# Kernel tuning notes

Hardware: AMD Instinct MI355X
Metric: run time of the kernel (lower is better)

## Reference

```python
import jax, jax.numpy as jnp
import numpy as np

DIM = 512
NUM_HEADS = 8
HEAD_DIM = DIM // NUM_HEADS
SCALE = HEAD_DIM ** -0.5
B, T = 8, 1024


def setup_inputs() -> dict:
    key = jax.random.key(0)
    ks = jax.random.split(key, 6)
    x = jax.random.normal(ks[0], (B, T, DIM), dtype=jnp.float32)
    attn_mask = jax.random.randint(ks[1], (B, T, T), 0, 2) == 1  # bool [B,T,T]
    s = 1.0 / np.sqrt(DIM)
    qkv_w = jax.random.uniform(ks[2], (3 * DIM, DIM), jnp.float32, -s, s)
    qkv_b = jax.random.uniform(ks[3], (3 * DIM,), jnp.float32, -s, s)
    proj_w = jax.random.uniform(ks[4], (DIM, DIM), jnp.float32, -s, s)
    proj_b = jax.random.uniform(ks[5], (DIM,), jnp.float32, -s, s)
    return {"x": x, "attn_mask": attn_mask, "qkv_w": qkv_w, "qkv_b": qkv_b,
            "proj_w": proj_w, "proj_b": proj_b}


def reference(x, attn_mask, qkv_w, qkv_b, proj_w, proj_b):
    b, t, c = x.shape
    # QKV projection (torch Linear: x @ W.T + b), split into q,k,v heads
    qkv = x @ qkv_w.T + qkv_b                      # [b,t,3*c]
    qkv = qkv.reshape(b, t, 3, NUM_HEADS, HEAD_DIM)
    qkv = jnp.transpose(qkv, (2, 0, 3, 1, 4))      # [3,b,h,t,d]
    q, k, v = qkv[0], qkv[1], qkv[2]
    scores = jnp.einsum('bhqd,bhkd->bhqk', q, k) * SCALE  # [b,h,t,t]
    min_val = jnp.finfo(scores.dtype).min
    scores = jnp.where(attn_mask[:, None, :, :], min_val, scores)
    attn = jax.nn.softmax(scores, axis=-1)
    out = jnp.einsum('bhqk,bhkd->bhqd', attn, v)   # [b,h,t,d]
    out = jnp.transpose(out, (0, 2, 1, 3)).reshape(b, t, c)
    return out @ proj_w.T + proj_b
```

## Files before the change

kernel.cpp:

```cpp
#include <hip/hip_runtime.h>
#include <math.h>

#define DIM   512
#define NH    8
#define HD    64
#define BATCH 8
#define SEQ   1024
#define QSCALE 0.18033688011112042f

typedef unsigned short u16;
typedef unsigned int   u32;
typedef unsigned long long u64;
typedef __bf16 bf16x8 __attribute__((ext_vector_type(8)));
typedef float  f32x4  __attribute__((ext_vector_type(4)));

__device__ inline u16 f2bf(float f) {
  u32 u = __builtin_bit_cast(u32, f);
  return (u16)((u + 0x7fffu + ((u >> 16) & 1u)) >> 16);
}
__device__ inline float bf2f(u16 h) {
  return __builtin_bit_cast(float, (u32)h << 16);
}
__device__ inline u32 pk2(float a, float b) {
  return (u32)f2bf(a) | ((u32)f2bf(b) << 16);
}

__device__ inline void a16(const u16* g, u16* l) {
  __builtin_amdgcn_global_load_lds(
      (const __attribute__((address_space(1))) u32*)g,
      (__attribute__((address_space(3))) u32*)l, 16, 0, 0);
}


__device__ inline void decomp_body(const float* __restrict__ src, u16* ph,
                                   u16* pl, int t) {
  #pragma unroll
  for (int c = 0; c < 4; ++c) {
    const int cid = c * 256 + t;
    const int row = cid & 15, kc = cid >> 4;
    float f[8];
    *(float4*)&f[0] = *(const float4*)&src[row * DIM + kc * 8];
    *(float4*)&f[4] = *(const float4*)&src[row * DIM + kc * 8 + 4];
    u16 hv[8], lv[8];
    #pragma unroll
    for (int j = 0; j < 8; ++j) {
      hv[j] = f2bf(f[j]);
      lv[j] = f2bf(f[j] - bf2f(hv[j]));
    }
    *(uint4*)&ph[(size_t)cid * 8] = *(const uint4*)hv;
    *(uint4*)&pl[(size_t)cid * 8] = *(const uint4*)lv;
  }
}

__global__ __launch_bounds__(256) void prep(
    const int* __restrict__ mask, u64* __restrict__ bits,
    const float* __restrict__ x, u16* __restrict__ xhi, u16* __restrict__ xlo,
    const float* __restrict__ qkvw, u16* __restrict__ wqh, u16* __restrict__ wql,
    const float* __restrict__ projw, u16* __restrict__ wph, u16* __restrict__ wpl) {
  const int blk = blockIdx.x;
  const int t = threadIdx.x;
  if (blk < 32768) {
    const size_t gid = (size_t)blk * 256 + t;
    const int lane = t & 63;
    const size_t w = gid >> 6;
    const int v = mask[w * 64 + lane];
    const u64 b = __ballot(v != 0);
    if (lane == 0) {
      const int bb = (int)(w >> 14), q = (int)((w >> 4) & 1023),
                kt = (int)(w & 15);
      bits[(((size_t)(bb << 4 | kt)) << 10) | q] = b;
    }
  } else if (blk < 33280) {
    const int rg = blk - 32768;
    decomp_body(x + (size_t)rg * 16 * DIM, xhi + (size_t)rg * 8192,
                xlo + (size_t)rg * 8192, t);
  } else if (blk < 33376) {
    const int rg = blk - 33280;
    decomp_body(qkvw + (size_t)rg * 16 * DIM, wqh + (size_t)rg * 8192,
                wql + (size_t)rg * 8192, t);
  } else {
    const int rg = blk - 33376;
    decomp_body(projw + (size_t)rg * 16 * DIM, wph + (size_t)rg * 8192,
                wpl + (size_t)rg * 8192, t);
  }
}

template <bool QKV>
__global__ __launch_bounds__(256) void mfma_gemm(
    const u16* __restrict__ Agh, const u16* __restrict__ Agl,
    const u16* __restrict__ Bgh, const u16* __restrict__ Bgl,
    const float* __restrict__ bias, void* __restrict__ out0,
    u16* __restrict__ kfr, u16* __restrict__ vfr) {
  __shared__ u16 sAh[4096];
  __shared__ u16 sAl[4096];
  __shared__ u16 sBh[4096];
  __shared__ u16 sBl[4096];

  const int tid = threadIdx.x;
  const int lane = tid & 63;
  const int wv = tid >> 6;
  const int lk = lane & 15, lq = lane >> 4;
  const int m0 = blockIdx.x * 128, n0 = blockIdx.y * 128;
  const int wm = (wv & 1) * 4;
  const int wn = (wv >> 1) * 4;

  const u16* gAh = Agh + (size_t)(m0 >> 4) * 8192 + lane * 8;
  const u16* gAl = Agl + (size_t)(m0 >> 4) * 8192 + lane * 8;
  const u16* gBh = Bgh + (size_t)(n0 >> 4) * 8192 + lane * 8;
  const u16* gBl = Bgl + (size_t)(n0 >> 4) * 8192 + lane * 8;

  f32x4 acc[4][4];
  #pragma unroll
  for (int i = 0; i < 4; ++i)
    #pragma unroll
    for (int j = 0; j < 4; ++j) acc[i][j] = (f32x4){0.f, 0.f, 0.f, 0.f};

  #pragma unroll 1
  for (int ki = 0; ki < 16; ++ki) {
    __syncthreads();
    #pragma unroll
    for (int it = 0; it < 2; ++it) {
      const int t = it * 4 + wv;
      const size_t go = (size_t)t * 8192 + ki * 512;
      const int lo_ = t * 512 + lane * 8;
      a16(gAh + go, &sAh[lo_]);
      a16(gAl + go, &sAl[lo_]);
      a16(gBh + go, &sBh[lo_]);
      a16(gBl + go, &sBl[lo_]);
    }
    __syncthreads();

    bf16x8 ah[4], al[4], bh[4], bl[4];
    #pragma unroll
    for (int i = 0; i < 4; ++i) {
      ah[i] = *(const bf16x8*)&sAh[(wm + i) * 512 + lane * 8];
      al[i] = *(const bf16x8*)&sAl[(wm + i) * 512 + lane * 8];
      bh[i] = *(const bf16x8*)&sBh[(wn + i) * 512 + lane * 8];
      bl[i] = *(const bf16x8*)&sBl[(wn + i) * 512 + lane * 8];
    }
    #pragma unroll
    for (int i = 0; i < 4; ++i)
      #pragma unroll
      for (int j = 0; j < 4; ++j) {
        acc[i][j] = __builtin_amdgcn_mfma_f32_16x16x32_bf16(ah[i], bh[j], acc[i][j], 0, 0, 0);
        acc[i][j] = __builtin_amdgcn_mfma_f32_16x16x32_bf16(ah[i], bl[j], acc[i][j], 0, 0, 0);
        acc[i][j] = __builtin_amdgcn_mfma_f32_16x16x32_bf16(al[i], bh[j], acc[i][j], 0, 0, 0);
      }
  }

  #pragma unroll
  for (int j = 0; j < 4; ++j) {
    const int n = n0 + (wn + j) * 16 + lk;
    const float bv_ = bias[n];
    #pragma unroll
    for (int i = 0; i < 4; ++i) {
      const int mb = m0 + (wm + i) * 16 + lq * 4;
      if (QKV) {
        const int which = n >> 9, h = (n >> 6) & 7, d = n & 63;
        const int b = mb >> 10, tok0 = mb & 1023;
        const size_t hb = (size_t)((b << 3) + h) << 16;
        if (which == 2) {
          const size_t base = hb + ((size_t)(tok0 >> 6) << 12) +
                              ((size_t)((d >> 4) & 3) << 10) +
                              ((size_t)((tok0 >> 5) & 1) << 9) +
                              ((size_t)((d & 15) + (((tok0 >> 3) & 3) << 4)) << 3) +
                              (size_t)(tok0 & 7);
          uint2 o2;
          o2.x = pk2(acc[i][j][0] + bv_, acc[i][j][1] + bv_);
          o2.y = pk2(acc[i][j][2] + bv_, acc[i][j][3] + bv_);
          *(uint2*)&vfr[base] = o2;
        } else if (which == 1) {
          const size_t base = hb + ((size_t)(tok0 >> 4) << 10) +
                              ((size_t)(d >> 5) << 9) + (size_t)(d & 7) +
                              ((size_t)(((d >> 3) & 3) << 4) << 3);
          #pragma unroll
          for (int r = 0; r < 4; ++r)
            kfr[base + (((tok0 & 15) + r) << 3)] = f2bf(acc[i][j][r] + bv_);
        } else {
          u16* dst = (u16*)out0;
          #pragma unroll
          for (int r = 0; r < 4; ++r)
            dst[(((size_t)((b << 3) + h) << 10 | (tok0 + r)) << 6) + d] =
                f2bf((acc[i][j][r] + bv_) * QSCALE);
        }
      } else {
        #pragma unroll
        for (int r = 0; r < 4; ++r)
          ((float*)out0)[(size_t)(mb + r) * DIM + n] = acc[i][j][r] + bv_;
      }
    }
  }
}

__global__ __launch_bounds__(256) void attn_mfma(
    const u16* __restrict__ qg, const u16* __restrict__ kfr,
    const u16* __restrict__ vfr, const u64* __restrict__ bitsT,
    u16* __restrict__ ohi, u16* __restrict__ olo) {
  __shared__ u16 Kls[4096];
  __shared__ u16 Vls[4096];
  __shared__ u16 Ps[64 * 72];

  const int tid = threadIdx.x;
  const int lane = tid & 63;
  const int wv = tid >> 6;
  const int lk = lane & 15, lq = lane >> 4;
  const int bh = blockIdx.x;
  const int q0 = blockIdx.y * 64;
  const int bb = bh >> 3;
  const int q = q0 + wv * 16 + lk;

  const u16* qrow = qg + ((size_t)(bh << 10 | q) << 6);
  const bf16x8 bq0 = *(const bf16x8*)(qrow + lq * 8);
  const bf16x8 bq1 = *(const bf16x8*)(qrow + 32 + lq * 8);

  const u16* kh = kfr + ((size_t)bh << 16);
  const u16* vh = vfr + ((size_t)bh << 16);
  const u64* bitp = bitsT + ((size_t)bb << 14) + q;
  u16* pw = &Ps[(wv * 16 + lk) * 72];

  f32x4 o_[4];
  float l = 0.f;
  #pragma unroll
  for (int t = 0; t < 4; ++t) o_[t] = (f32x4){0.f, 0.f, 0.f, 0.f};

  #pragma unroll 1
  for (int kt = 0; kt < 16; ++kt) {
    __syncthreads();
    #pragma unroll
    for (int it = 0; it < 2; ++it) {
      const int c = it * 4 + wv;
      const int off = c * 512 + lane * 8;
      a16(kh + (size_t)(kt << 12) + off, &Kls[off]);
      a16(vh + (size_t)(kt << 12) + off, &Vls[off]);
    }
    const u64 wd = bitp[kt << 10];
    __syncthreads();

    f32x4 st[4];
    const f32x4 z4 = (f32x4){0.f, 0.f, 0.f, 0.f};
    #pragma unroll
    for (int t = 0; t < 4; ++t) {
      const bf16x8 ak0 = *(const bf16x8*)&Kls[t * 1024 + lane * 8];
      const bf16x8 ak1 = *(const bf16x8*)&Kls[t * 1024 + 512 + lane * 8];
      f32x4 a = __builtin_amdgcn_mfma_f32_16x16x32_bf16(ak0, bq0, z4, 0, 0, 0);
      st[t] = __builtin_amdgcn_mfma_f32_16x16x32_bf16(ak1, bq1, a, 0, 0, 0);
    }

    const u32 w0 = (u32)wd, w1 = (u32)(wd >> 32);
    #pragma unroll
    for (int t = 0; t < 4; ++t) {
      const u32 w = (t < 2) ? w0 : w1;
      const int base = (t & 1) * 16 + lq * 4;
      float p[4];
      #pragma unroll
      for (int r = 0; r < 4; ++r) {
        const float sv = ((w >> (base + r)) & 1u) ? -INFINITY : st[t][r];
        p[r] = __builtin_amdgcn_exp2f(sv);
        l += p[r];
      }
      *(uint2*)(pw + t * 16 + lq * 4) = uint2{pk2(p[0], p[1]), pk2(p[2], p[3])};
    }

    const bf16x8 pa0 = *(const bf16x8*)(pw + lq * 8);
    const bf16x8 pa1 = *(const bf16x8*)(pw + 32 + lq * 8);
    #pragma unroll
    for (int t = 0; t < 4; ++t) {
      const bf16x8 vb0 = *(const bf16x8*)&Vls[t * 1024 + lane * 8];
      const bf16x8 vb1 = *(const bf16x8*)&Vls[t * 1024 + 512 + lane * 8];
      o_[t] = __builtin_amdgcn_mfma_f32_16x16x32_bf16(pa0, vb0, o_[t], 0, 0, 0);
      o_[t] = __builtin_amdgcn_mfma_f32_16x16x32_bf16(pa1, vb1, o_[t], 0, 0, 0);
    }
  }

  l += __shfl_xor(l, 16);
  l += __shfl_xor(l, 32);

  const int h = bh & 7;
  #pragma unroll
  for (int r = 0; r < 4; ++r) {
    const float inv = 1.0f / __shfl(l, lq * 4 + r);
    const int tok = q0 + wv * 16 + lq * 4 + r;
    const int m = (bb << 10) | tok;
    const size_t rgo = (size_t)(m >> 4) * 8192 + (size_t)(m & 15) * 8;
    #pragma unroll
    for (int t = 0; t < 4; ++t) {
      const int d = t * 16 + lk;
      const int k = (h << 6) | d;
      const float v = o_[t][r] * inv;
      const u16 hv = f2bf(v);
      const size_t off = rgo + (size_t)(k >> 3) * 128 + (k & 7);
      ohi[off] = hv;
      olo[off] = f2bf(v - bf2f(hv));
    }
  }
}

extern "C" void kernel_launch(void* const* d_in, const int* in_sizes, int n_in,
                              void* d_out, int out_size, void* d_ws,
                              size_t ws_size, hipStream_t stream) {
  const float* x      = (const float*)d_in[0];
  const int*   mask   = (const int*)d_in[1];
  const float* qkv_w  = (const float*)d_in[2];
  const float* qkv_b  = (const float*)d_in[3];
  const float* proj_w = (const float*)d_in[4];
  const float* proj_b = (const float*)d_in[5];
  float* out = (float*)d_out;

  const size_t SZ = (size_t)BATCH * NH * SEQ * HD;
  u64* bits = (u64*)d_ws;
  u16* qb  = (u16*)(bits + 131072);
  u16* kfr = qb + SZ;
  u16* vfr = kfr + SZ;
  u16* xhi = vfr + SZ;
  u16* xlo = xhi + SZ;
  u16* ohi = xlo + SZ;
  u16* olo = ohi + SZ;
  u16* wqh = olo + SZ;
  u16* wql = wqh + 1536 * 512;
  u16* wph = wql + 1536 * 512;
  u16* wpl = wph + 512 * 512;

  prep<<<33408, 256, 0, stream>>>(mask, bits, x, xhi, xlo,
                                  qkv_w, wqh, wql, proj_w, wph, wpl);
  mfma_gemm<true><<<dim3(64, 12), 256, 0, stream>>>(
      xhi, xlo, wqh, wql, qkv_b, qb, kfr, vfr);
  attn_mfma<<<dim3(64, SEQ / 64), 256, 0, stream>>>(
      qb, kfr, vfr, bits, ohi, olo);
  mfma_gemm<false><<<dim3(64, 4), 256, 0, stream>>>(
      ohi, olo, wph, wpl, proj_b, out, nullptr, nullptr);
}
```

Baseline: 214.6 us.

## Double-buffer LDS tiles in GEMM and attention kernels to overlap loads

Both the split-bf16 GEMM and the attention kernel now use two LDS buffers and prefetch the next K-tile while computing on the current one. This removes one barrier per iteration and hides global-to-LDS latency behind the MFMA work. MFMA sections are also wrapped in s_setprio so matrix work is favoured across waves. LDS use doubles (64KB in the GEMM), which may cut the number of resident blocks per CU, and the attention kernel now holds more fragments in registers.

```diff
diff --git a/kernel.cpp b/kernel.cpp
--- a/kernel.cpp
+++ b/kernel.cpp
@@ -91,10 +91,10 @@
     const u16* __restrict__ Bgh, const u16* __restrict__ Bgl,
     const float* __restrict__ bias, void* __restrict__ out0,
     u16* __restrict__ kfr, u16* __restrict__ vfr) {
-  __shared__ u16 sAh[4096];
-  __shared__ u16 sAl[4096];
-  __shared__ u16 sBh[4096];
-  __shared__ u16 sBl[4096];
+  __shared__ u16 sAh[2][4096];
+  __shared__ u16 sAl[2][4096];
+  __shared__ u16 sBh[2][4096];
+  __shared__ u16 sBl[2][4096];
 
   const int tid = threadIdx.x;
   const int lane = tid & 63;
@@ -109,35 +109,43 @@
   const u16* gBh = Bgh + (size_t)(n0 >> 4) * 8192 + lane * 8;
   const u16* gBl = Bgl + (size_t)(n0 >> 4) * 8192 + lane * 8;
 
+  auto stage = [&](int bufi, int ki) {
+    #pragma unroll
+    for (int it = 0; it < 2; ++it) {
+      const int t = it * 4 + wv;
+      const size_t go = (size_t)t * 8192 + (size_t)ki * 512;
+      const int lo_ = t * 512 + lane * 8;
+      a16(gAh + go, &sAh[bufi][lo_]);
+      a16(gAl + go, &sAl[bufi][lo_]);
+      a16(gBh + go, &sBh[bufi][lo_]);
+      a16(gBl + go, &sBl[bufi][lo_]);
+    }
+  };
+
   f32x4 acc[4][4];
   #pragma unroll
   for (int i = 0; i < 4; ++i)
     #pragma unroll
     for (int j = 0; j < 4; ++j) acc[i][j] = (f32x4){0.f, 0.f, 0.f, 0.f};
+
+  stage(0, 0);
+  __syncthreads();
 
   #pragma unroll 1
   for (int ki = 0; ki < 16; ++ki) {
-    __syncthreads();
-    #pragma unroll
-    for (int it = 0; it < 2; ++it) {
-      const int t = it * 4 + wv;
-      const size_t go = (size_t)t * 8192 + ki * 512;
-      const int lo_ = t * 512 + lane * 8;
-      a16(gAh + go, &sAh[lo_]);
-      a16(gAl + go, &sAl[lo_]);
-      a16(gBh + go, &sBh[lo_]);
-      a16(gBl + go, &sBl[lo_]);
-    }
-    __syncthreads();
-
+    const int cur = ki & 1;
     bf16x8 ah[4], al[4], bh[4], bl[4];
     #pragma unroll
     for (int i = 0; i < 4; ++i) {
-      ah[i] = *(const bf16x8*)&sAh[(wm + i) * 512 + lane * 8];
-      al[i] = *(const bf16x8*)&sAl[(wm + i) * 512 + lane * 8];
-      bh[i] = *(const bf16x8*)&sBh[(wn + i) * 512 + lane * 8];
-      bl[i] = *(const bf16x8*)&sBl[(wn + i) * 512 + lane * 8];
-    }
+      ah[i] = *(const bf16x8*)&sAh[cur][(wm + i) * 512 + lane * 8];
+      al[i] = *(const bf16x8*)&sAl[cur][(wm + i) * 512 + lane * 8];
+      bh[i] = *(const bf16x8*)&sBh[cur][(wn + i) * 512 + lane * 8];
+      bl[i] = *(const bf16x8*)&sBl[cur][(wn + i) * 512 + lane * 8];
+    }
+    if (ki < 15) stage(cur ^ 1, ki + 1);
+    __builtin_amdgcn_sched_barrier(0);
+
+    __builtin_amdgcn_s_setprio(1);
     #pragma unroll
     for (int i = 0; i < 4; ++i)
       #pragma unroll
@@ -146,6 +154,9 @@
         acc[i][j] = __builtin_amdgcn_mfma_f32_16x16x32_bf16(ah[i], bl[j], acc[i][j], 0, 0, 0);
         acc[i][j] = __builtin_amdgcn_mfma_f32_16x16x32_bf16(al[i], bh[j], acc[i][j], 0, 0, 0);
       }
+    __builtin_amdgcn_s_setprio(0);
+
+    __syncthreads();
   }
 
   #pragma unroll
@@ -196,8 +207,8 @@
     const u16* __restrict__ qg, const u16* __restrict__ kfr,
     const u16* __restrict__ vfr, const u64* __restrict__ bitsT,
     u16* __restrict__ ohi, u16* __restrict__ olo) {
-  __shared__ u16 Kls[4096];
-  __shared__ u16 Vls[4096];
+  __shared__ u16 Kls[2][4096];
+  __shared__ u16 Vls[2][4096];
   __shared__ u16 Ps[64 * 72];
 
   const int tid = threadIdx.x;
@@ -218,33 +229,49 @@
   const u64* bitp = bitsT + ((size_t)bb << 14) + q;
   u16* pw = &Ps[(wv * 16 + lk) * 72];
 
-  f32x4 o_[4];
-  float l = 0.f;
-  #pragma unroll
-  for (int t = 0; t < 4; ++t) o_[t] = (f32x4){0.f, 0.f, 0.f, 0.f};
-
-  #pragma unroll 1
-  for (int kt = 0; kt < 16; ++kt) {
-    __syncthreads();
+  auto stage = [&](int bufi, int kt) {
     #pragma unroll
     for (int it = 0; it < 2; ++it) {
       const int c = it * 4 + wv;
       const int off = c * 512 + lane * 8;
-      a16(kh + (size_t)(kt << 12) + off, &Kls[off]);
-      a16(vh + (size_t)(kt << 12) + off, &Vls[off]);
-    }
-    const u64 wd = bitp[kt << 10];
-    __syncthreads();
+      a16(kh + ((size_t)kt << 12) + off, &Kls[bufi][off]);
+      a16(vh + ((size_t)kt << 12) + off, &Vls[bufi][off]);
+    }
+  };
+
+  f32x4 o_[4];
+  float l = 0.f;
+  #pragma unroll
+  for (int t = 0; t < 4; ++t) o_[t] = (f32x4){0.f, 0.f, 0.f, 0.f};
+
+  stage(0, 0);
+  __syncthreads();
+
+  #pragma unroll 1
+  for (int kt = 0; kt < 16; ++kt) {
+    const int cur = kt & 1;
+    const u64 wd = bitp[(size_t)kt << 10];
+
+    bf16x8 ak0[4], ak1[4], vb0[4], vb1[4];
+    #pragma unroll
+    for (int t = 0; t < 4; ++t) {
+      ak0[t] = *(const bf16x8*)&Kls[cur][t * 1024 + lane * 8];
+      ak1[t] = *(const bf16x8*)&Kls[cur][t * 1024 + 512 + lane * 8];
+      vb0[t] = *(const bf16x8*)&Vls[cur][t * 1024 + lane * 8];
+      vb1[t] = *(const bf16x8*)&Vls[cur][t * 1024 + 512 + lane * 8];
+    }
+    if (kt < 15) stage(cur ^ 1, kt + 1);
+    __builtin_amdgcn_sched_barrier(0);
 
     f32x4 st[4];
     const f32x4 z4 = (f32x4){0.f, 0.f, 0.f, 0.f};
-    #pragma unroll
-    for (int t = 0; t < 4; ++t) {
-      const bf16x8 ak0 = *(const bf16x8*)&Kls[t * 1024 + lane * 8];
-      const bf16x8 ak1 = *(const bf16x8*)&Kls[t * 1024 + 512 + lane * 8];
-      f32x4 a = __builtin_amdgcn_mfma_f32_16x16x32_bf16(ak0, bq0, z4, 0, 0, 0);
-      st[t] = __builtin_amdgcn_mfma_f32_16x16x32_bf16(ak1, bq1, a, 0, 0, 0);
-    }
+    __builtin_amdgcn_s_setprio(1);
+    #pragma unroll
+    for (int t = 0; t < 4; ++t) {
+      f32x4 a = __builtin_amdgcn_mfma_f32_16x16x32_bf16(ak0[t], bq0, z4, 0, 0, 0);
+      st[t] = __builtin_amdgcn_mfma_f32_16x16x32_bf16(ak1[t], bq1, a, 0, 0, 0);
+    }
+    __builtin_amdgcn_s_setprio(0);
 
     const u32 w0 = (u32)wd, w1 = (u32)(wd >> 32);
     #pragma unroll
@@ -263,13 +290,15 @@
 
     const bf16x8 pa0 = *(const bf16x8*)(pw + lq * 8);
     const bf16x8 pa1 = *(const bf16x8*)(pw + 32 + lq * 8);
-    #pragma unroll
-    for (int t = 0; t < 4; ++t) {
-      const bf16x8 vb0 = *(const bf16x8*)&Vls[t * 1024 + lane * 8];
-      const bf16x8 vb1 = *(const bf16x8*)&Vls[t * 1024 + 512 + lane * 8];
-      o_[t] = __builtin_amdgcn_mfma_f32_16x16x32_bf16(pa0, vb0, o_[t], 0, 0, 0);
-      o_[t] = __builtin_amdgcn_mfma_f32_16x16x32_bf16(pa1, vb1, o_[t], 0, 0, 0);
-    }
+    __builtin_amdgcn_s_setprio(1);
+    #pragma unroll
+    for (int t = 0; t < 4; ++t) {
+      o_[t] = __builtin_amdgcn_mfma_f32_16x16x32_bf16(pa0, vb0[t], o_[t], 0, 0, 0);
+      o_[t] = __builtin_amdgcn_mfma_f32_16x16x32_bf16(pa1, vb1[t], o_[t], 0, 0, 0);
+    }
+    __builtin_amdgcn_s_setprio(0);
+
+    __syncthreads();
   }
 
   l += __shfl_xor(l, 16);
```

After: 205.8 us. 1.04x faster.
